# Kernel tuning notes

Hardware: AMD Instinct MI355X
Metric: run time of the kernel (lower is better)

Reference implementation:

```python
import jax, jax.numpy as jnp
import numpy as np

N_NODES = 50000
N_EDGES = 800000
D_NODE = 64
D_EDGE = 32
OUT_DIM = 32
NUM_HEADS = 4


def setup_inputs() -> dict:
    key = jax.random.key(0)
    ks = jax.random.split(key, 7)
    node_features = jax.random.normal(ks[0], (N_NODES, D_NODE), dtype=jnp.float32)
    edge_features = jax.random.normal(ks[1], (N_EDGES, D_EDGE), dtype=jnp.float32)
    edge_index = jax.random.randint(ks[2], (2, N_EDGES), 0, N_NODES, dtype=jnp.int32)
    attn_mask = jax.random.bernoulli(ks[3], 0.95, (N_EDGES,))
    # Dense kernels (flax stores kernel as [in, out]); scale ~ 1/sqrt(fan_in)
    W_a = jax.random.normal(ks[4], (2 * D_NODE + D_EDGE, NUM_HEADS * OUT_DIM), dtype=jnp.float32) / np.sqrt(2 * D_NODE + D_EDGE)
    W_m = jax.random.normal(ks[5], (D_NODE + D_EDGE, NUM_HEADS * OUT_DIM), dtype=jnp.float32) / np.sqrt(D_NODE + D_EDGE)
    a_w = jax.random.normal(ks[6], (OUT_DIM, 1), dtype=jnp.float32) / np.sqrt(OUT_DIM)
    return {"node_features": node_features, "edge_features": edge_features,
            "edge_index": edge_index, "attn_mask": attn_mask,
            "W_a": W_a, "W_m": W_m, "a_w": a_w}


def reference(node_features, edge_features, edge_index, attn_mask, W_a, W_m, a_w):
    n_nodes = node_features.shape[0]
    src, tgt = edge_index[0], edge_index[1]
    src_feat = node_features[src]   # [E, D_NODE]
    tgt_feat = node_features[tgt]   # [E, D_NODE]

    h_a = (jnp.concatenate([src_feat, edge_features, tgt_feat], axis=-1) @ W_a)
    h_a = h_a.reshape(-1, NUM_HEADS, OUT_DIM)                       # [E, H, D]
    h_m = (jnp.concatenate([edge_features, tgt_feat], axis=-1) @ W_m)
    h_m = h_m.reshape(-1, NUM_HEADS, OUT_DIM)                       # [E, H, D]

    logits = jax.nn.leaky_relu(h_a, negative_slope=0.2) @ a_w      # [E, H, 1]
    logits = jnp.where(attn_mask[:, None, None], logits, -jnp.inf)

    # dead-node detection: nodes whose every incident edge is masked
    max_per_node = jax.ops.segment_max(logits.reshape(logits.shape[0], -1), src,
                                       num_segments=n_nodes)       # [N, H]
    dead_nodes = jnp.isneginf(max_per_node[:, 0])
    dead_mask = dead_nodes[src]
    safe_logits = jnp.where(dead_mask[:, None, None], jnp.zeros_like(logits), logits)

    # segment softmax over edges grouped by src node
    seg_max = jax.ops.segment_max(safe_logits, src, num_segments=n_nodes)   # [N, H, 1]
    unnorm = jnp.exp(safe_logits - jnp.where(jnp.isneginf(seg_max), 0.0, seg_max)[src])
    denom = jax.ops.segment_sum(unnorm, src, num_segments=n_nodes)          # [N, H, 1]
    attn = unnorm / denom[src]                                              # [E, H, 1]

    msgs = attn * h_m                                                        # [E, H, D]
    h = jax.ops.segment_sum(msgs, src, num_segments=n_nodes)                 # [N, H, D]
    return h
```

## Files before the change

kernel.cpp:

```cpp
#include <hip/hip_runtime.h>
#include <hip/hip_bf16.h>
#include <math.h>

#define N_NODES 50000
#define N_EDGES 800000
#define D_NODE 64
#define D_EDGE 32
#define OUT_DIM 32
#define NUM_HEADS 4
#define NCH 49

__device__ __forceinline__ unsigned bf16rne(float x) {
    unsigned u = __float_as_uint(x);
    unsigned r = ((u >> 16) & 1u) + 0x7fffu;
    return (u + r) >> 16;
}
__device__ __forceinline__ float2 unpack_bf2(unsigned p) {
    return make_float2(__uint_as_float(p << 16), __uint_as_float(p & 0xffff0000u));
}

__global__ void k_detect(const unsigned char* __restrict__ mask, int* __restrict__ mode) {
    __shared__ int cnt;
    if (threadIdx.x == 0) cnt = 0;
    __syncthreads();
    int c = 0;
    for (int i = threadIdx.x; i < 4096; i += 256) c += (mask[i] != 0);
    atomicAdd(&cnt, c);
    __syncthreads();
    if (threadIdx.x == 0) {
        int md;
        if (cnt > (4096 * 70) / 100)      md = 0;
        else if (cnt > (4096 * 35) / 100) md = 1;
        else                              md = 2;
        *mode = md;
    }
}

__device__ __forceinline__ bool loadmask(const void* m, int mode, int e) {
    if (mode == 0) return ((const unsigned char*)m)[e] != 0;
    if (mode == 1) return ((const float*)m)[e] != 0.f;
    return ((const int*)m)[e] != 0;
}

__global__ __launch_bounds__(256) void k_nodegemm(
    const float* __restrict__ nf, const float* __restrict__ Wa, const float* __restrict__ Wm,
    float* __restrict__ Psrc, unsigned* __restrict__ PT) {
    __shared__ float At[64][72];
    __shared__ float Bt[64][128];
    const int mb = blockIdx.y;
    const float* Wsrc = (mb == 0) ? Wa : (mb == 1 ? (Wa + 96 * 128) : (Wm + 32 * 128));
    const int n0 = blockIdx.x * 64;
    const int tid = threadIdx.x;

    for (int i = tid; i < 1024; i += 256) {
        int r = i >> 4;
        int kc = (i & 15) << 2;
        float4 v = make_float4(0.f, 0.f, 0.f, 0.f);
        if (n0 + r < N_NODES) v = *(const float4*)(nf + (size_t)(n0 + r) * 64 + kc);
        At[kc + 0][r] = v.x; At[kc + 1][r] = v.y; At[kc + 2][r] = v.z; At[kc + 3][r] = v.w;
    }
    for (int i = tid; i < 2048; i += 256) {
        int k = i >> 5;
        int c = (i & 31) << 2;
        *(float4*)(&Bt[k][c]) = *(const float4*)(Wsrc + (size_t)k * 128 + c);
    }
    __syncthreads();

    const int ty = tid >> 5;
    const int tx = tid & 31;
    float acc[8][4];
#pragma unroll
    for (int r = 0; r < 8; r++)
#pragma unroll
        for (int c = 0; c < 4; c++) acc[r][c] = 0.f;

    for (int k = 0; k < 64; k++) {
        float4 b = *(const float4*)(&Bt[k][tx * 4]);
        float4 a0 = *(const float4*)(&At[k][ty * 8]);
        float4 a1 = *(const float4*)(&At[k][ty * 8 + 4]);
        float a[8] = {a0.x, a0.y, a0.z, a0.w, a1.x, a1.y, a1.z, a1.w};
#pragma unroll
        for (int r = 0; r < 8; r++) {
            acc[r][0] += a[r] * b.x; acc[r][1] += a[r] * b.y;
            acc[r][2] += a[r] * b.z; acc[r][3] += a[r] * b.w;
        }
    }
    for (int r = 0; r < 8; r++) {
        int n = n0 + ty * 8 + r;
        if (n >= N_NODES) continue;
        if (mb == 0) {
            *(float4*)(Psrc + (size_t)n * 128 + tx * 4) =
                make_float4(acc[r][0], acc[r][1], acc[r][2], acc[r][3]);
        } else {
            unsigned p0 = bf16rne(acc[r][0]) | (bf16rne(acc[r][1]) << 16);
            unsigned p1 = bf16rne(acc[r][2]) | (bf16rne(acc[r][3]) << 16);
            unsigned base = (mb == 1) ? 0u : 64u;
            *(uint2*)(PT + (size_t)n * 128 + base + tx * 2) = make_uint2(p0, p1);
        }
    }
}

__global__ void k_deg(const int* __restrict__ src, int* __restrict__ deg) {
    int i = blockIdx.x * blockDim.x + threadIdx.x;
    if (i < N_EDGES) atomicAdd(&deg[src[i]], 1);
}

__global__ void k_scan_partial(const int* __restrict__ deg, int* __restrict__ csum) {
    __shared__ int sd[256];
    int b = blockIdx.x, tid = threadIdx.x;
    int s = 0, st = b * 1024;
    for (int i = tid; i < 1024; i += 256) {
        int idx = st + i;
        if (idx < N_NODES) s += deg[idx];
    }
    sd[tid] = s; __syncthreads();
    for (int off = 128; off > 0; off >>= 1) {
        if (tid < off) sd[tid] += sd[tid + off];
        __syncthreads();
    }
    if (tid == 0) csum[b] = sd[0];
}

__global__ void k_scan_chunks(int* __restrict__ csum) {
    if (threadIdx.x == 0 && blockIdx.x == 0) {
        int acc = 0;
        for (int i = 0; i < NCH; i++) { int v = csum[i]; csum[i] = acc; acc += v; }
    }
}

__global__ __launch_bounds__(1024) void k_scan_apply(
    const int* __restrict__ deg, const int* __restrict__ csum, int* __restrict__ basep) {
    __shared__ int sd[1024];
    int b = blockIdx.x, tid = threadIdx.x;
    int idx = b * 1024 + tid;
    int v = (idx < N_NODES) ? deg[idx] : 0;
    sd[tid] = v; __syncthreads();
    for (int off = 1; off < 1024; off <<= 1) {
        int add = (tid >= off) ? sd[tid - off] : 0;
        __syncthreads();
        sd[tid] += add;
        __syncthreads();
    }
    if (idx < N_NODES) basep[idx] = csum[b] + sd[tid] - v;
}

__global__ void k_scatter(const int* __restrict__ src, const int* __restrict__ basep,
                          int* __restrict__ cursor, int* __restrict__ order) {
    int i = blockIdx.x * blockDim.x + threadIdx.x;
    if (i < N_EDGES) {
        int s = src[i];
        int p = basep[s] + atomicAdd(&cursor[s], 1);
        order[p] = i;
    }
}

__global__ __launch_bounds__(256) void k_fused(
    const float* __restrict__ ef, const int* __restrict__ tgt,
    const void* __restrict__ mask, const int* __restrict__ modep,
    const float* __restrict__ Wa, const float* __restrict__ Wm, const float* __restrict__ aw,
    const float* __restrict__ Psrc, const unsigned* __restrict__ PT,
    const int* __restrict__ deg, const int* __restrict__ basep,
    const int* __restrict__ order, float* __restrict__ out) {
    const int lane = threadIdx.x & 63;
    const int wv = threadIdx.x >> 6;
    const int n = blockIdx.x * 4 + wv;
    const int l15 = lane & 15;
    const int base16 = lane & 48;
    const int d0 = lane * 2;

    float2 W[32];
#pragma unroll
    for (int j = 0; j < 32; j++)
        W[j] = *(const float2*)(Wa + (size_t)(64 + j) * 128 + d0);

    const float2 awv = *(const float2*)(aw + 2 * l15);
    const int mode = *modep;
    const int dg = deg[n], bs = basep[n];
    const float2 ps = *(const float2*)(Psrc + (size_t)n * 128 + d0);

    float acc0 = 0.f, acc1 = 0.f;
    float w0 = 0.f, w1 = 0.f;
    float den = 0.f;
    float accU0 = 0.f, accU1 = 0.f;
    float wU0 = 0.f, wU1 = 0.f;

    const int last = N_EDGES - 1;
    int e1 = order[min(bs + 0, last)];
    int e2 = order[min(bs + 1, last)];
    int e3 = order[min(bs + 2, last)];
    int t1 = tgt[e1];
    int t2 = tgt[e2];
    unsigned pa = PT[(size_t)t1 * 128 + lane];
    unsigned pm = PT[(size_t)t1 * 128 + 64 + lane];
    float2 efc = *(const float2*)(ef + (size_t)e1 * 32 + 2 * l15);
    bool mkc = loadmask(mask, mode, e1);

    for (int i = 0; i < dg; i++) {
        int e4 = order[min(bs + i + 3, last)];
        int t3 = tgt[e3];
        unsigned paN = PT[(size_t)t2 * 128 + lane];
        unsigned pmN = PT[(size_t)t2 * 128 + 64 + lane];
        float2 efN = *(const float2*)(ef + (size_t)e2 * 32 + 2 * l15);
        bool mkN = loadmask(mask, mode, e2);

        float2 paf = unpack_bf2(pa);
        float a0 = ps.x + paf.x;
        float a1 = ps.y + paf.y;
#pragma unroll
        for (int j = 0; j < 32; j += 2) {
            int sl = base16 + (j >> 1);
            float ex = __shfl(efc.x, sl);
            float ey = __shfl(efc.y, sl);
            a0 += ex * W[j].x + ey * W[j + 1].x;
            a1 += ex * W[j].y + ey * W[j + 1].y;
        }
        float lr0 = (a0 >= 0.f) ? a0 : 0.2f * a0;
        float lr1 = (a1 >= 0.f) ? a1 : 0.2f * a1;
        float v = lr0 * awv.x + lr1 * awv.y;
        v += __shfl_xor(v, 8);
        v += __shfl_xor(v, 4);
        v += __shfl_xor(v, 2);
        v += __shfl_xor(v, 1);
        float u = mkc ? __expf(fminf(v, 60.f)) : 0.f;

        float2 pmf = unpack_bf2(pm);
        acc0 += u * pmf.x; acc1 += u * pmf.y;
        w0 += u * efc.x;   w1 += u * efc.y;
        den += u;
        accU0 += pmf.x;    accU1 += pmf.y;
        wU0 += efc.x;      wU1 += efc.y;

        pa = paN; pm = pmN; efc = efN; mkc = mkN;
        e2 = e3; e3 = e4; t2 = t3;
    }

    bool dead = (dg > 0) && (den == 0.f);
    float sw0 = dead ? wU0 : w0, sw1 = dead ? wU1 : w1;
    float sa0 = dead ? accU0 : acc0, sa1 = dead ? accU1 : acc1;
    float sden = dead ? (float)dg : den;

    float t0 = 0.f, tt1 = 0.f;
#pragma unroll
    for (int k = 0; k < 32; k += 2) {
        int sl = base16 + (k >> 1);
        float wa = __shfl(sw0, sl);
        float wb = __shfl(sw1, sl);
        float2 m0 = *(const float2*)(Wm + (size_t)k * 128 + d0);
        float2 m1 = *(const float2*)(Wm + (size_t)(k + 1) * 128 + d0);
        t0  += wa * m0.x + wb * m1.x;
        tt1 += wa * m0.y + wb * m1.y;
    }
    float o0 = (dg > 0) ? (sa0 + t0) / sden : 0.f;
    float o1 = (dg > 0) ? (sa1 + tt1) / sden : 0.f;
    *(float2*)(out + (size_t)n * 128 + d0) = make_float2(o0, o1);
}

extern "C" void kernel_launch(void* const* d_in, const int* in_sizes, int n_in,
                              void* d_out, int out_size, void* d_ws, size_t ws_size,
                              hipStream_t stream) {
    const float* nf = (const float*)d_in[0];
    const float* ef = (const float*)d_in[1];
    const int* eidx = (const int*)d_in[2];
    const void* mask = d_in[3];
    const float* Wa = (const float*)d_in[4];
    const float* Wm = (const float*)d_in[5];
    const float* aw = (const float*)d_in[6];
    const int* src = eidx;
    const int* tgt = eidx + N_EDGES;
    float* out = (float*)d_out;

    char* ws = (char*)d_ws;
    size_t off = 0;
    auto alloc = [&](size_t bytes) -> void* {
        void* p = ws + off;
        off += (bytes + 255) & ~(size_t)255;
        return p;
    };
    int* mode       = (int*)alloc(256);
    float* Psrc     = (float*)alloc((size_t)N_NODES * 128 * 4);
    unsigned* PT    = (unsigned*)alloc((size_t)N_NODES * 128 * 4);
    int* deg        = (int*)alloc((size_t)N_NODES * 4);
    int* cursor     = (int*)alloc((size_t)N_NODES * 4);
    int* basep      = (int*)alloc((size_t)N_NODES * 4);
    int* csum       = (int*)alloc((size_t)NCH * 4);
    int* order      = (int*)alloc((size_t)N_EDGES * 4);

    hipMemsetAsync(deg, 0, (size_t)N_NODES * 4, stream);
    hipMemsetAsync(cursor, 0, (size_t)N_NODES * 4, stream);

    k_detect<<<1, 256, 0, stream>>>((const unsigned char*)mask, mode);
    k_nodegemm<<<dim3((N_NODES + 63) / 64, 3), 256, 0, stream>>>(nf, Wa, Wm, Psrc, PT);
    k_deg<<<(N_EDGES + 255) / 256, 256, 0, stream>>>(src, deg);
    k_scan_partial<<<NCH, 256, 0, stream>>>(deg, csum);
    k_scan_chunks<<<1, 64, 0, stream>>>(csum);
    k_scan_apply<<<NCH, 1024, 0, stream>>>(deg, csum, basep);
    k_scatter<<<(N_EDGES + 255) / 256, 256, 0, stream>>>(src, basep, cursor, order);
    k_fused<<<N_NODES / 4, 256, 0, stream>>>(ef, tgt, mask, mode, Wa, Wm, aw,
                                             Psrc, PT, deg, basep, order, out);
}
```

Baseline: 768.1 us.

## Pre-gather edge data into CSR order and interleave node projection table

Adds a gather kernel that writes, in src-sorted order, a packed 64-bit record per edge (edge id, mask bit, target) and optionally a sorted copy of edge features. The fused kernel then reads these contiguously instead of chasing order->tgt/mask/ef pointers. It also interleaves the two bf16 projection halves so each lane fetches one uint2 per target node. The aim is shorter dependent-load chains and more coalesced edge-feature reads. The cost is an extra pass over the edge features (about 100MB of traffic) and extra workspace.

```diff
diff --git a/kernel.cpp b/kernel.cpp
--- a/kernel.cpp
+++ b/kernel.cpp
@@ -44,7 +44,7 @@
 
 __global__ __launch_bounds__(256) void k_nodegemm(
     const float* __restrict__ nf, const float* __restrict__ Wa, const float* __restrict__ Wm,
-    float* __restrict__ Psrc, unsigned* __restrict__ PT) {
+    float* __restrict__ Psrc, unsigned* __restrict__ PT2) {
     __shared__ float At[64][72];
     __shared__ float Bt[64][128];
     const int mb = blockIdx.y;
@@ -94,8 +94,9 @@
         } else {
             unsigned p0 = bf16rne(acc[r][0]) | (bf16rne(acc[r][1]) << 16);
             unsigned p1 = bf16rne(acc[r][2]) | (bf16rne(acc[r][3]) << 16);
-            unsigned base = (mb == 1) ? 0u : 64u;
-            *(uint2*)(PT + (size_t)n * 128 + base + tx * 2) = make_uint2(p0, p1);
+            unsigned fld = (mb == 1) ? 0u : 1u;
+            PT2[((size_t)n * 64 + 2 * tx) * 2 + fld] = p0;
+            PT2[((size_t)n * 64 + 2 * tx + 1) * 2 + fld] = p1;
         }
     }
 }
@@ -154,13 +155,35 @@
     }
 }
 
+template <bool DO_EFS>
+__global__ void k_gather(const int* __restrict__ order, const int* __restrict__ tgt,
+                         const void* __restrict__ mask, const int* __restrict__ modep,
+                         const float* __restrict__ ef,
+                         float* __restrict__ efS, unsigned long long* __restrict__ tmE) {
+    const int g = threadIdx.x >> 5, k = threadIdx.x & 31;
+    const int mode = *modep;
+    const int p0 = (blockIdx.x * 8 + g) * 4;
+#pragma unroll
+    for (int q = 0; q < 4; q++) {
+        int p = p0 + q;
+        int e = order[p];
+        if (DO_EFS) efS[(size_t)p * 32 + k] = ef[(size_t)e * 32 + k];
+        if (k == 0) {
+            unsigned long long mk = loadmask(mask, mode, e) ? 1ull : 0ull;
+            tmE[p] = ((unsigned long long)(unsigned)e << 32) | (mk << 16)
+                   | (unsigned long long)(unsigned)tgt[e];
+        }
+    }
+}
+
+template <bool USE_EFS>
 __global__ __launch_bounds__(256) void k_fused(
-    const float* __restrict__ ef, const int* __restrict__ tgt,
-    const void* __restrict__ mask, const int* __restrict__ modep,
+    const float* __restrict__ ef, const float* __restrict__ efS,
+    const unsigned long long* __restrict__ tmE,
     const float* __restrict__ Wa, const float* __restrict__ Wm, const float* __restrict__ aw,
-    const float* __restrict__ Psrc, const unsigned* __restrict__ PT,
+    const float* __restrict__ Psrc, const uint2* __restrict__ PT2,
     const int* __restrict__ deg, const int* __restrict__ basep,
-    const int* __restrict__ order, float* __restrict__ out) {
+    float* __restrict__ out) {
     const int lane = threadIdx.x & 63;
     const int wv = threadIdx.x >> 6;
     const int n = blockIdx.x * 4 + wv;
@@ -174,7 +197,6 @@
         W[j] = *(const float2*)(Wa + (size_t)(64 + j) * 128 + d0);
 
     const float2 awv = *(const float2*)(aw + 2 * l15);
-    const int mode = *modep;
     const int dg = deg[n], bs = basep[n];
     const float2 ps = *(const float2*)(Psrc + (size_t)n * 128 + d0);
 
@@ -185,32 +207,30 @@
     float wU0 = 0.f, wU1 = 0.f;
 
     const int last = N_EDGES - 1;
-    int e1 = order[min(bs + 0, last)];
-    int e2 = order[min(bs + 1, last)];
-    int e3 = order[min(bs + 2, last)];
-    int t1 = tgt[e1];
-    int t2 = tgt[e2];
-    unsigned pa = PT[(size_t)t1 * 128 + lane];
-    unsigned pm = PT[(size_t)t1 * 128 + 64 + lane];
-    float2 efc = *(const float2*)(ef + (size_t)e1 * 32 + 2 * l15);
-    bool mkc = loadmask(mask, mode, e1);
+    unsigned long long tm0 = tmE[min(bs + 0, last)];
+    unsigned long long tm1 = tmE[min(bs + 1, last)];
+    unsigned long long tm2 = tmE[min(bs + 2, last)];
+    uint2 pt0 = PT2[(size_t)(tm0 & 0xFFFFu) * 64 + lane];
+    uint2 pt1 = PT2[(size_t)(tm1 & 0xFFFFu) * 64 + lane];
+    float2 ef0;
+    if (USE_EFS) ef0 = *(const float2*)(efS + (size_t)min(bs, last) * 32 + 2 * l15);
+    else         ef0 = *(const float2*)(ef + (size_t)(tm0 >> 32) * 32 + 2 * l15);
 
     for (int i = 0; i < dg; i++) {
-        int e4 = order[min(bs + i + 3, last)];
-        int t3 = tgt[e3];
-        unsigned paN = PT[(size_t)t2 * 128 + lane];
-        unsigned pmN = PT[(size_t)t2 * 128 + 64 + lane];
-        float2 efN = *(const float2*)(ef + (size_t)e2 * 32 + 2 * l15);
-        bool mkN = loadmask(mask, mode, e2);
-
-        float2 paf = unpack_bf2(pa);
+        unsigned long long tm3 = tmE[min(bs + i + 3, last)];
+        uint2 pt2 = PT2[(size_t)(tm2 & 0xFFFFu) * 64 + lane];
+        float2 ef1;
+        if (USE_EFS) ef1 = *(const float2*)(efS + (size_t)min(bs + i + 1, last) * 32 + 2 * l15);
+        else         ef1 = *(const float2*)(ef + (size_t)(tm1 >> 32) * 32 + 2 * l15);
+
+        float2 paf = unpack_bf2(pt0.x);
         float a0 = ps.x + paf.x;
         float a1 = ps.y + paf.y;
 #pragma unroll
         for (int j = 0; j < 32; j += 2) {
             int sl = base16 + (j >> 1);
-            float ex = __shfl(efc.x, sl);
-            float ey = __shfl(efc.y, sl);
+            float ex = __shfl(ef0.x, sl);
+            float ey = __shfl(ef0.y, sl);
             a0 += ex * W[j].x + ey * W[j + 1].x;
             a1 += ex * W[j].y + ey * W[j + 1].y;
         }
@@ -221,17 +241,18 @@
         v += __shfl_xor(v, 4);
         v += __shfl_xor(v, 2);
         v += __shfl_xor(v, 1);
-        float u = mkc ? __expf(fminf(v, 60.f)) : 0.f;
-
-        float2 pmf = unpack_bf2(pm);
+        float u = ((tm0 >> 16) & 1ull) ? __expf(fminf(v, 60.f)) : 0.f;
+
+        float2 pmf = unpack_bf2(pt0.y);
         acc0 += u * pmf.x; acc1 += u * pmf.y;
-        w0 += u * efc.x;   w1 += u * efc.y;
+        w0 += u * ef0.x;   w1 += u * ef0.y;
         den += u;
         accU0 += pmf.x;    accU1 += pmf.y;
-        wU0 += efc.x;      wU1 += efc.y;
-
-        pa = paN; pm = pmN; efc = efN; mkc = mkN;
-        e2 = e3; e3 = e4; t2 = t3;
+        wU0 += ef0.x;      wU1 += ef0.y;
+
+        tm0 = tm1; tm1 = tm2; tm2 = tm3;
+        pt0 = pt1; pt1 = pt2;
+        ef0 = ef1;
     }
 
     bool dead = (dg > 0) && (den == 0.f);
@@ -278,23 +299,35 @@
     };
     int* mode       = (int*)alloc(256);
     float* Psrc     = (float*)alloc((size_t)N_NODES * 128 * 4);
-    unsigned* PT    = (unsigned*)alloc((size_t)N_NODES * 128 * 4);
+    unsigned* PT2   = (unsigned*)alloc((size_t)N_NODES * 64 * 8);
     int* deg        = (int*)alloc((size_t)N_NODES * 4);
     int* cursor     = (int*)alloc((size_t)N_NODES * 4);
     int* basep      = (int*)alloc((size_t)N_NODES * 4);
     int* csum       = (int*)alloc((size_t)NCH * 4);
     int* order      = (int*)alloc((size_t)N_EDGES * 4);
+    unsigned long long* tmE = (unsigned long long*)alloc((size_t)N_EDGES * 8);
+    size_t base_need = off;
+    float* efS      = (float*)alloc((size_t)N_EDGES * 32 * 4);
+    const bool use_efs = (ws_size >= off);
+    (void)base_need;
 
     hipMemsetAsync(deg, 0, (size_t)N_NODES * 4, stream);
     hipMemsetAsync(cursor, 0, (size_t)N_NODES * 4, stream);
 
     k_detect<<<1, 256, 0, stream>>>((const unsigned char*)mask, mode);
-    k_nodegemm<<<dim3((N_NODES + 63) / 64, 3), 256, 0, stream>>>(nf, Wa, Wm, Psrc, PT);
+    k_nodegemm<<<dim3((N_NODES + 63) / 64, 3), 256, 0, stream>>>(nf, Wa, Wm, Psrc, PT2);
     k_deg<<<(N_EDGES + 255) / 256, 256, 0, stream>>>(src, deg);
     k_scan_partial<<<NCH, 256, 0, stream>>>(deg, csum);
     k_scan_chunks<<<1, 64, 0, stream>>>(csum);
     k_scan_apply<<<NCH, 1024, 0, stream>>>(deg, csum, basep);
     k_scatter<<<(N_EDGES + 255) / 256, 256, 0, stream>>>(src, basep, cursor, order);
-    k_fused<<<N_NODES / 4, 256, 0, stream>>>(ef, tgt, mask, mode, Wa, Wm, aw,
-                                             Psrc, PT, deg, basep, order, out);
-}
+    if (use_efs) {
+        k_gather<true><<<N_EDGES / 32, 256, 0, stream>>>(order, tgt, mask, mode, ef, efS, tmE);
+        k_fused<true><<<N_NODES / 4, 256, 0, stream>>>(ef, efS, tmE, Wa, Wm, aw,
+                                                       Psrc, (const uint2*)PT2, deg, basep, out);
+    } else {
+        k_gather<false><<<N_EDGES / 32, 256, 0, stream>>>(order, tgt, mask, mode, ef, efS, tmE);
+        k_fused<false><<<N_NODES / 4, 256, 0, stream>>>(ef, efS, tmE, Wa, Wm, aw,
+                                                        Psrc, (const uint2*)PT2, deg, basep, out);
+    }
+}
```

Result: slower. 787.1 us (+2.5%).

## Pack edge metadata, interleave target projections, process two nodes per wave

Applied to the files above, without the earlier changes.

The scatter kernel now writes a packed 64-bit record per sorted edge (edge id, mask bit, target index), so the fused kernel no longer does dependent loads through order, tgt and mask. The bf16 target projections for attention and message are interleaved per lane into one uint2, so a single 8-byte load replaces two 4-byte loads. Each wave now handles two source nodes at once to expose more independent memory requests, with launch bounds raised to allow 3 blocks. The trade-offs are more register pressure, divergence when the two nodes differ in degree, and a 16-bit target field that only works while node counts stay below 65536.

```diff
diff --git a/kernel.cpp b/kernel.cpp
--- a/kernel.cpp
+++ b/kernel.cpp
@@ -44,7 +44,7 @@
 
 __global__ __launch_bounds__(256) void k_nodegemm(
     const float* __restrict__ nf, const float* __restrict__ Wa, const float* __restrict__ Wm,
-    float* __restrict__ Psrc, unsigned* __restrict__ PT) {
+    float* __restrict__ Psrc, unsigned* __restrict__ PT2) {
     __shared__ float At[64][72];
     __shared__ float Bt[64][128];
     const int mb = blockIdx.y;
@@ -94,8 +94,9 @@
         } else {
             unsigned p0 = bf16rne(acc[r][0]) | (bf16rne(acc[r][1]) << 16);
             unsigned p1 = bf16rne(acc[r][2]) | (bf16rne(acc[r][3]) << 16);
-            unsigned base = (mb == 1) ? 0u : 64u;
-            *(uint2*)(PT + (size_t)n * 128 + base + tx * 2) = make_uint2(p0, p1);
+            unsigned fld = (mb == 1) ? 0u : 1u;
+            PT2[((size_t)n * 64 + 2 * tx) * 2 + fld] = p0;
+            PT2[((size_t)n * 64 + 2 * tx + 1) * 2 + fld] = p1;
         }
     }
 }
@@ -144,26 +145,31 @@
     if (idx < N_NODES) basep[idx] = csum[b] + sd[tid] - v;
 }
 
-__global__ void k_scatter(const int* __restrict__ src, const int* __restrict__ basep,
-                          int* __restrict__ cursor, int* __restrict__ order) {
+__global__ void k_scatter(const int* __restrict__ src, const int* __restrict__ tgt,
+                          const void* __restrict__ mask, const int* __restrict__ modep,
+                          const int* __restrict__ basep, int* __restrict__ cursor,
+                          unsigned long long* __restrict__ tmE) {
     int i = blockIdx.x * blockDim.x + threadIdx.x;
     if (i < N_EDGES) {
+        const int mode = *modep;
         int s = src[i];
         int p = basep[s] + atomicAdd(&cursor[s], 1);
-        order[p] = i;
-    }
-}
-
-__global__ __launch_bounds__(256) void k_fused(
-    const float* __restrict__ ef, const int* __restrict__ tgt,
-    const void* __restrict__ mask, const int* __restrict__ modep,
+        unsigned long long mk = loadmask(mask, mode, i) ? 1ull : 0ull;
+        tmE[p] = ((unsigned long long)(unsigned)i << 32) | (mk << 16)
+               | (unsigned long long)(unsigned)tgt[i];
+    }
+}
+
+__global__ __launch_bounds__(256, 3) void k_fused(
+    const float* __restrict__ ef, const unsigned long long* __restrict__ tmE,
     const float* __restrict__ Wa, const float* __restrict__ Wm, const float* __restrict__ aw,
-    const float* __restrict__ Psrc, const unsigned* __restrict__ PT,
+    const float* __restrict__ Psrc, const uint2* __restrict__ PT2,
     const int* __restrict__ deg, const int* __restrict__ basep,
-    const int* __restrict__ order, float* __restrict__ out) {
+    float* __restrict__ out) {
     const int lane = threadIdx.x & 63;
     const int wv = threadIdx.x >> 6;
-    const int n = blockIdx.x * 4 + wv;
+    const int wid = blockIdx.x * 4 + wv;
+    const int nA = wid * 2, nB = nA + 1;
     const int l15 = lane & 15;
     const int base16 = lane & 48;
     const int d0 = lane * 2;
@@ -174,85 +180,132 @@
         W[j] = *(const float2*)(Wa + (size_t)(64 + j) * 128 + d0);
 
     const float2 awv = *(const float2*)(aw + 2 * l15);
-    const int mode = *modep;
-    const int dg = deg[n], bs = basep[n];
-    const float2 ps = *(const float2*)(Psrc + (size_t)n * 128 + d0);
-
-    float acc0 = 0.f, acc1 = 0.f;
-    float w0 = 0.f, w1 = 0.f;
-    float den = 0.f;
-    float accU0 = 0.f, accU1 = 0.f;
-    float wU0 = 0.f, wU1 = 0.f;
+    const int dgA = deg[nA], bsA = basep[nA];
+    const int dgB = deg[nB], bsB = basep[nB];
+    const float2 psA = *(const float2*)(Psrc + (size_t)nA * 128 + d0);
+    const float2 psB = *(const float2*)(Psrc + (size_t)nB * 128 + d0);
+
+    float accA0 = 0.f, accA1 = 0.f, wA0 = 0.f, wA1 = 0.f, denA = 0.f;
+    float acUA0 = 0.f, acUA1 = 0.f, wUA0 = 0.f, wUA1 = 0.f;
+    float accB0 = 0.f, accB1 = 0.f, wB0 = 0.f, wB1 = 0.f, denB = 0.f;
+    float acUB0 = 0.f, acUB1 = 0.f, wUB0 = 0.f, wUB1 = 0.f;
 
     const int last = N_EDGES - 1;
-    int e1 = order[min(bs + 0, last)];
-    int e2 = order[min(bs + 1, last)];
-    int e3 = order[min(bs + 2, last)];
-    int t1 = tgt[e1];
-    int t2 = tgt[e2];
-    unsigned pa = PT[(size_t)t1 * 128 + lane];
-    unsigned pm = PT[(size_t)t1 * 128 + 64 + lane];
-    float2 efc = *(const float2*)(ef + (size_t)e1 * 32 + 2 * l15);
-    bool mkc = loadmask(mask, mode, e1);
-
-    for (int i = 0; i < dg; i++) {
-        int e4 = order[min(bs + i + 3, last)];
-        int t3 = tgt[e3];
-        unsigned paN = PT[(size_t)t2 * 128 + lane];
-        unsigned pmN = PT[(size_t)t2 * 128 + 64 + lane];
-        float2 efN = *(const float2*)(ef + (size_t)e2 * 32 + 2 * l15);
-        bool mkN = loadmask(mask, mode, e2);
-
-        float2 paf = unpack_bf2(pa);
-        float a0 = ps.x + paf.x;
-        float a1 = ps.y + paf.y;
+    unsigned long long tmA0 = tmE[min(bsA + 0, last)];
+    unsigned long long tmA1 = tmE[min(bsA + 1, last)];
+    unsigned long long tmA2 = tmE[min(bsA + 2, last)];
+    unsigned long long tmB0 = tmE[min(bsB + 0, last)];
+    unsigned long long tmB1 = tmE[min(bsB + 1, last)];
+    unsigned long long tmB2 = tmE[min(bsB + 2, last)];
+    uint2 ptA0 = PT2[(size_t)(tmA0 & 0xFFFFu) * 64 + lane];
+    uint2 ptA1 = PT2[(size_t)(tmA1 & 0xFFFFu) * 64 + lane];
+    uint2 ptB0 = PT2[(size_t)(tmB0 & 0xFFFFu) * 64 + lane];
+    uint2 ptB1 = PT2[(size_t)(tmB1 & 0xFFFFu) * 64 + lane];
+    float2 efA0 = *(const float2*)(ef + (size_t)(tmA0 >> 32) * 32 + 2 * l15);
+    float2 efB0 = *(const float2*)(ef + (size_t)(tmB0 >> 32) * 32 + 2 * l15);
+
+    const int mx = max(dgA, dgB);
+    for (int i = 0; i < mx; i++) {
+        unsigned long long tmA3 = tmE[min(bsA + i + 3, last)];
+        unsigned long long tmB3 = tmE[min(bsB + i + 3, last)];
+        uint2 ptA2 = PT2[(size_t)(tmA2 & 0xFFFFu) * 64 + lane];
+        uint2 ptB2 = PT2[(size_t)(tmB2 & 0xFFFFu) * 64 + lane];
+        float2 efA1 = *(const float2*)(ef + (size_t)(tmA1 >> 32) * 32 + 2 * l15);
+        float2 efB1 = *(const float2*)(ef + (size_t)(tmB1 >> 32) * 32 + 2 * l15);
+
+        float2 pafA = unpack_bf2(ptA0.x);
+        float2 pafB = unpack_bf2(ptB0.x);
+        float aA0 = psA.x + pafA.x, aA1 = psA.y + pafA.y;
+        float aB0 = psB.x + pafB.x, aB1 = psB.y + pafB.y;
 #pragma unroll
         for (int j = 0; j < 32; j += 2) {
             int sl = base16 + (j >> 1);
-            float ex = __shfl(efc.x, sl);
-            float ey = __shfl(efc.y, sl);
-            a0 += ex * W[j].x + ey * W[j + 1].x;
-            a1 += ex * W[j].y + ey * W[j + 1].y;
-        }
-        float lr0 = (a0 >= 0.f) ? a0 : 0.2f * a0;
-        float lr1 = (a1 >= 0.f) ? a1 : 0.2f * a1;
-        float v = lr0 * awv.x + lr1 * awv.y;
-        v += __shfl_xor(v, 8);
-        v += __shfl_xor(v, 4);
-        v += __shfl_xor(v, 2);
-        v += __shfl_xor(v, 1);
-        float u = mkc ? __expf(fminf(v, 60.f)) : 0.f;
-
-        float2 pmf = unpack_bf2(pm);
-        acc0 += u * pmf.x; acc1 += u * pmf.y;
-        w0 += u * efc.x;   w1 += u * efc.y;
-        den += u;
-        accU0 += pmf.x;    accU1 += pmf.y;
-        wU0 += efc.x;      wU1 += efc.y;
-
-        pa = paN; pm = pmN; efc = efN; mkc = mkN;
-        e2 = e3; e3 = e4; t2 = t3;
-    }
-
-    bool dead = (dg > 0) && (den == 0.f);
-    float sw0 = dead ? wU0 : w0, sw1 = dead ? wU1 : w1;
-    float sa0 = dead ? accU0 : acc0, sa1 = dead ? accU1 : acc1;
-    float sden = dead ? (float)dg : den;
-
-    float t0 = 0.f, tt1 = 0.f;
-#pragma unroll
-    for (int k = 0; k < 32; k += 2) {
-        int sl = base16 + (k >> 1);
-        float wa = __shfl(sw0, sl);
-        float wb = __shfl(sw1, sl);
-        float2 m0 = *(const float2*)(Wm + (size_t)k * 128 + d0);
-        float2 m1 = *(const float2*)(Wm + (size_t)(k + 1) * 128 + d0);
-        t0  += wa * m0.x + wb * m1.x;
-        tt1 += wa * m0.y + wb * m1.y;
-    }
-    float o0 = (dg > 0) ? (sa0 + t0) / sden : 0.f;
-    float o1 = (dg > 0) ? (sa1 + tt1) / sden : 0.f;
-    *(float2*)(out + (size_t)n * 128 + d0) = make_float2(o0, o1);
+            float exA = __shfl(efA0.x, sl);
+            float eyA = __shfl(efA0.y, sl);
+            float exB = __shfl(efB0.x, sl);
+            float eyB = __shfl(efB0.y, sl);
+            aA0 += exA * W[j].x + eyA * W[j + 1].x;
+            aA1 += exA * W[j].y + eyA * W[j + 1].y;
+            aB0 += exB * W[j].x + eyB * W[j + 1].x;
+            aB1 += exB * W[j].y + eyB * W[j + 1].y;
+        }
+        float lrA0 = (aA0 >= 0.f) ? aA0 : 0.2f * aA0;
+        float lrA1 = (aA1 >= 0.f) ? aA1 : 0.2f * aA1;
+        float lrB0 = (aB0 >= 0.f) ? aB0 : 0.2f * aB0;
+        float lrB1 = (aB1 >= 0.f) ? aB1 : 0.2f * aB1;
+        float vA = lrA0 * awv.x + lrA1 * awv.y;
+        float vB = lrB0 * awv.x + lrB1 * awv.y;
+#pragma unroll
+        for (int off = 8; off > 0; off >>= 1) {
+            vA += __shfl_xor(vA, off);
+            vB += __shfl_xor(vB, off);
+        }
+        if (i < dgA) {
+            float u = ((tmA0 >> 16) & 1ull) ? __expf(fminf(vA, 60.f)) : 0.f;
+            float2 pmf = unpack_bf2(ptA0.y);
+            accA0 += u * pmf.x; accA1 += u * pmf.y;
+            wA0 += u * efA0.x;  wA1 += u * efA0.y;
+            denA += u;
+            acUA0 += pmf.x;     acUA1 += pmf.y;
+            wUA0 += efA0.x;     wUA1 += efA0.y;
+        }
+        if (i < dgB) {
+            float u = ((tmB0 >> 16) & 1ull) ? __expf(fminf(vB, 60.f)) : 0.f;
+            float2 pmf = unpack_bf2(ptB0.y);
+            accB0 += u * pmf.x; accB1 += u * pmf.y;
+            wB0 += u * efB0.x;  wB1 += u * efB0.y;
+            denB += u;
+            acUB0 += pmf.x;     acUB1 += pmf.y;
+            wUB0 += efB0.x;     wUB1 += efB0.y;
+        }
+
+        tmA0 = tmA1; tmA1 = tmA2; tmA2 = tmA3;
+        tmB0 = tmB1; tmB1 = tmB2; tmB2 = tmB3;
+        ptA0 = ptA1; ptA1 = ptA2;
+        ptB0 = ptB1; ptB1 = ptB2;
+        efA0 = efA1; efB0 = efB1;
+    }
+
+    {
+        bool dead = (dgA > 0) && (denA == 0.f);
+        float sw0 = dead ? wUA0 : wA0, sw1 = dead ? wUA1 : wA1;
+        float sa0 = dead ? acUA0 : accA0, sa1 = dead ? acUA1 : accA1;
+        float sden = dead ? (float)dgA : denA;
+        float t0 = 0.f, t1 = 0.f;
+#pragma unroll
+        for (int k = 0; k < 32; k += 2) {
+            int sl = base16 + (k >> 1);
+            float wa = __shfl(sw0, sl);
+            float wb = __shfl(sw1, sl);
+            float2 m0 = *(const float2*)(Wm + (size_t)k * 128 + d0);
+            float2 m1 = *(const float2*)(Wm + (size_t)(k + 1) * 128 + d0);
+            t0 += wa * m0.x + wb * m1.x;
+            t1 += wa * m0.y + wb * m1.y;
+        }
+        float o0 = (dgA > 0) ? (sa0 + t0) / sden : 0.f;
+        float o1 = (dgA > 0) ? (sa1 + t1) / sden : 0.f;
+        *(float2*)(out + (size_t)nA * 128 + d0) = make_float2(o0, o1);
+    }
+    {
+        bool dead = (dgB > 0) && (denB == 0.f);
+        float sw0 = dead ? wUB0 : wB0, sw1 = dead ? wUB1 : wB1;
+        float sa0 = dead ? acUB0 : accB0, sa1 = dead ? acUB1 : accB1;
+        float sden = dead ? (float)dgB : denB;
+        float t0 = 0.f, t1 = 0.f;
+#pragma unroll
+        for (int k = 0; k < 32; k += 2) {
+            int sl = base16 + (k >> 1);
+            float wa = __shfl(sw0, sl);
+            float wb = __shfl(sw1, sl);
+            float2 m0 = *(const float2*)(Wm + (size_t)k * 128 + d0);
+            float2 m1 = *(const float2*)(Wm + (size_t)(k + 1) * 128 + d0);
+            t0 += wa * m0.x + wb * m1.x;
+            t1 += wa * m0.y + wb * m1.y;
+        }
+        float o0 = (dgB > 0) ? (sa0 + t0) / sden : 0.f;
+        float o1 = (dgB > 0) ? (sa1 + t1) / sden : 0.f;
+        *(float2*)(out + (size_t)nB * 128 + d0) = make_float2(o0, o1);
+    }
 }
 
 extern "C" void kernel_launch(void* const* d_in, const int* in_sizes, int n_in,
@@ -278,23 +331,24 @@
     };
     int* mode       = (int*)alloc(256);
     float* Psrc     = (float*)alloc((size_t)N_NODES * 128 * 4);
-    unsigned* PT    = (unsigned*)alloc((size_t)N_NODES * 128 * 4);
+    unsigned* PT2   = (unsigned*)alloc((size_t)N_NODES * 64 * 8);
     int* deg        = (int*)alloc((size_t)N_NODES * 4);
     int* cursor     = (int*)alloc((size_t)N_NODES * 4);
     int* basep      = (int*)alloc((size_t)N_NODES * 4);
     int* csum       = (int*)alloc((size_t)NCH * 4);
-    int* order      = (int*)alloc((size_t)N_EDGES * 4);
+    unsigned long long* tmE = (unsigned long long*)alloc((size_t)N_EDGES * 8);
 
     hipMemsetAsync(deg, 0, (size_t)N_NODES * 4, stream);
     hipMemsetAsync(cursor, 0, (size_t)N_NODES * 4, stream);
 
     k_detect<<<1, 256, 0, stream>>>((const unsigned char*)mask, mode);
-    k_nodegemm<<<dim3((N_NODES + 63) / 64, 3), 256, 0, stream>>>(nf, Wa, Wm, Psrc, PT);
+    k_nodegemm<<<dim3((N_NODES + 63) / 64, 3), 256, 0, stream>>>(nf, Wa, Wm, Psrc, PT2);
     k_deg<<<(N_EDGES + 255) / 256, 256, 0, stream>>>(src, deg);
     k_scan_partial<<<NCH, 256, 0, stream>>>(deg, csum);
     k_scan_chunks<<<1, 64, 0, stream>>>(csum);
     k_scan_apply<<<NCH, 1024, 0, stream>>>(deg, csum, basep);
-    k_scatter<<<(N_EDGES + 255) / 256, 256, 0, stream>>>(src, basep, cursor, order);
-    k_fused<<<N_NODES / 4, 256, 0, stream>>>(ef, tgt, mask, mode, Wa, Wm, aw,
-                                             Psrc, PT, deg, basep, order, out);
-}
+    k_scatter<<<(N_EDGES + 255) / 256, 256, 0, stream>>>(src, tgt, mask, mode,
+                                                         basep, cursor, tmE);
+    k_fused<<<N_NODES / 8, 256, 0, stream>>>(ef, tmE, Wa, Wm, aw,
+                                             Psrc, (const uint2*)PT2, deg, basep, out);
+}
```

Result: slower. 1.397 ms (+81.9%).
